# Kernel optimization log

Measured on AMD Instinct MI355X. Metric: run time of the kernel, lower is better.

The kernel has to match this reference:

```python
import jax, jax.numpy as jnp
import numpy as np

NEG_INF = -1e30


def setup_inputs() -> dict:
    B, N, D = 512, 256, 256
    key = jax.random.key(0)
    ks = jax.random.split(key, 10)
    s = 1.0 / np.sqrt(D)
    return {
        "enc": jax.random.normal(ks[0], (B, N, D), dtype=jnp.float32),
        "init_token": jax.random.normal(ks[1], (D,), dtype=jnp.float32),
        "w_ih": jax.random.uniform(ks[2], (3 * D, D), minval=-s, maxval=s, dtype=jnp.float32),
        "w_hh": jax.random.uniform(ks[3], (3 * D, D), minval=-s, maxval=s, dtype=jnp.float32),
        "b_ih": jax.random.uniform(ks[4], (3 * D,), minval=-s, maxval=s, dtype=jnp.float32),
        "b_hh": jax.random.uniform(ks[5], (3 * D,), minval=-s, maxval=s, dtype=jnp.float32),
        "wq": jax.random.uniform(ks[6], (D, D), minval=-s, maxval=s, dtype=jnp.float32),
        "bq": jax.random.uniform(ks[7], (D,), minval=-s, maxval=s, dtype=jnp.float32),
        "wk": jax.random.uniform(ks[8], (D, D), minval=-s, maxval=s, dtype=jnp.float32),
        "bk": jax.random.uniform(ks[9], (D,), minval=-s, maxval=s, dtype=jnp.float32),
    }


def gru_cell(x, h, w_ih, w_hh, b_ih, b_hh):
    # torch.nn.GRUCell math; gates packed as [reset, update, new]
    gi = x @ w_ih.T + b_ih          # [B, 3D]
    gh = h @ w_hh.T + b_hh          # [B, 3D]
    D = h.shape[-1]
    i_r, i_z, i_n = gi[:, :D], gi[:, D:2 * D], gi[:, 2 * D:]
    h_r, h_z, h_n = gh[:, :D], gh[:, D:2 * D], gh[:, 2 * D:]
    r = jax.nn.sigmoid(i_r + h_r)
    z = jax.nn.sigmoid(i_z + h_z)
    n = jnp.tanh(i_n + r * h_n)
    return (1.0 - z) * n + z * h


def pointer_decode(enc, init_token, w_ih, w_hh, b_ih, b_hh, wq, bq, wk, bk):
    # Greedy decode (deterministic analogue of decode_type='greedy').
    B, N, D = enc.shape
    scale = 1.0 / np.sqrt(D)
    keys = enc @ wk.T + bk                         # [B, N, D]
    rows = jnp.arange(B)

    def step(carry, _):
        state, prev_embed, mask = carry
        state = gru_cell(prev_embed, state, w_ih, w_hh, b_ih, b_hh)   # [B, D]
        query = state @ wq.T + bq                                     # [B, D]
        logits = jnp.einsum('bd,bnd->bn', query, keys) * scale        # [B, N]
        logits = jnp.where(mask, logits, NEG_INF)
        logp = jax.nn.log_softmax(logits, axis=-1)                    # [B, N]
        probs = jnp.exp(logp)
        entropy = -jnp.sum(probs * jnp.where(mask, logp, 0.0), axis=-1)  # [B]
        idx = jnp.argmax(probs, axis=-1)                              # [B]
        step_logp = logp[rows, idx]                                   # [B]
        prev_embed = enc[rows, idx]                                   # [B, D]
        mask = mask.at[rows, idx].set(False)
        return (state, prev_embed, mask), (idx, step_logp, entropy)

    carry0 = (enc.mean(axis=1),
              jnp.broadcast_to(init_token, (B, D)),
              jnp.ones((B, N), dtype=bool))
    _, (tours, logps, ents) = jax.lax.scan(step, carry0, None, length=N)
    return tours.T, logps.T, ents.T  # each [B, N]


def reference(enc, init_token, w_ih, w_hh, b_ih, b_hh, wq, bq, wk, bk):
    return pointer_decode(enc, init_token, w_ih, w_hh, b_ih, b_hh, wq, bq, wk, bk)
```

## Files before the change

kernel.cpp:

```cpp
#include <hip/hip_runtime.h>

#define B_ 512
#define N_ 256
#define D_ 256
#define NEGINF (-1e30)

typedef float v4f __attribute__((ext_vector_type(4)));

__global__ void transpose_k(const float* __restrict__ in, float* __restrict__ out,
                            int R, int C) {
  __shared__ float tile[32][33];
  int rb = blockIdx.y * 32, cb = blockIdx.x * 32;
  int tx = threadIdx.x, ty = threadIdx.y;
  for (int i = ty; i < 32; i += 8) {
    int r = rb + i, c = cb + tx;
    if (r < R && c < C) tile[i][tx] = in[r * C + c];
  }
  __syncthreads();
  for (int i = ty; i < 32; i += 8) {
    int c = cb + i, r = rb + tx;
    if (r < R && c < C) out[c * R + r] = tile[tx][i];
  }
}

__global__ __launch_bounds__(256) void packW_k(const float* __restrict__ in,
                                               float* __restrict__ out) {
  int idx = blockIdx.x * 256 + threadIdx.x;
  int j = idx >> 6, c4 = idx & 63;
  int g = j >> 8, o = j & 255;
  int w16 = o >> 4, k = c4 & 15, l = 4 * (o & 15) + (c4 >> 4);
  ((v4f*)out)[((w16 * 16 + k) * 3 + g) * 64 + l] = ((const v4f*)in)[idx];
}

__global__ __launch_bounds__(256) void wqk_k(const float* __restrict__ wk,
                                             const float* __restrict__ wq,
                                             const float* __restrict__ bq,
                                             double* __restrict__ WqkP,
                                             double* __restrict__ bqk) {
  int c = blockIdx.x, e = threadIdx.x;
  double acc = 0.0;
  for (int dd = 0; dd < 256; ++dd)
    acc += (double)wk[dd * 256 + c] * (double)wq[dd * 256 + e];
  int w16 = c >> 4, k2 = (e >> 1) & 31, l = 4 * (c & 15) + (e >> 6), comp = e & 1;
  WqkP[(size_t)(((w16 * 32) + k2) * 64 + l) * 2 + comp] = acc;
  if (e == 0) {
    double s = 0.0;
    for (int dd = 0; dd < 256; ++dd) s += (double)wk[dd * 256 + c] * (double)bq[dd];
    bqk[c] = s;
  }
}

__global__ __launch_bounds__(256) void encp_k(const float* __restrict__ enc,
                                              float* __restrict__ encP) {
  int b = blockIdx.y;
  int idx = blockIdx.x * 256 + threadIdx.x;
  int l = idx & 63, rest = idx >> 6;
  int k = rest & 15, w16 = rest >> 4;
  int n = w16 * 16 + (l >> 2), c4 = (l & 3) * 16 + k;
  ((v4f*)encP)[(size_t)b * 16384 + idx] =
      *(const v4f*)(enc + (size_t)b * 65536 + n * 256 + c4 * 4);
}

__global__ __launch_bounds__(768) void gi_k(const float* __restrict__ enc,
                                            const float* __restrict__ wihT,
                                            const float* __restrict__ b_ih,
                                            double* __restrict__ Gi) {
  int b = blockIdx.x, j = threadIdx.x;
  __shared__ float encS[32][256];
  const float* encB = enc + (size_t)b * 65536;
  double bias = (double)b_ih[j];
  for (int n0 = 0; n0 < 256; n0 += 32) {
    __syncthreads();
    for (int i = j; i < 2048; i += 768)
      ((float4*)encS)[i] = ((const float4*)(encB + n0 * 256))[i];
    __syncthreads();
    double acc[32];
#pragma unroll
    for (int jj = 0; jj < 32; ++jj) acc[jj] = bias;
    for (int c0 = 0; c0 < 256; c0 += 4) {
      double w0 = (double)wihT[(c0 + 0) * 768 + j];
      double w1 = (double)wihT[(c0 + 1) * 768 + j];
      double w2 = (double)wihT[(c0 + 2) * 768 + j];
      double w3 = (double)wihT[(c0 + 3) * 768 + j];
#pragma unroll
      for (int jj = 0; jj < 32; ++jj) {
        const float4 e = *(const float4*)&encS[jj][c0];
        acc[jj] += w0 * (double)e.x + w1 * (double)e.y + w2 * (double)e.z + w3 * (double)e.w;
      }
    }
#pragma unroll
    for (int jj = 0; jj < 32; ++jj)
      Gi[((size_t)b * 256 + n0 + jj) * 768 + j] = acc[jj];
  }
}

template <bool USE_GI>
__global__ __launch_bounds__(1024, 4) void decode_k(
    const float* __restrict__ enc, const float* __restrict__ init_token,
    const float* __restrict__ b_ih, const float* __restrict__ b_hh,
    const float* __restrict__ wihP, const float* __restrict__ whhP,
    const double* __restrict__ WqkP, const double* __restrict__ bqk,
    const float* __restrict__ encP, const double* __restrict__ Gi,
    float* __restrict__ out) {
  const int tid = threadIdx.x;
  const int WV = tid >> 6;
  const int LN = tid & 63;
  const int O = WV * 16 + (LN >> 2);
  const int S = LN & 3;
  const int ROW = S >> 1;
  const int b0 = blockIdx.x * 2;

  __shared__ alignas(16) double hS[2][2][D_];
  __shared__ alignas(16) double xS[2][D_];
  __shared__ alignas(16) double giS[2][768];
  __shared__ alignas(16) double qs[2][D_];
  __shared__ double lg[2][N_];
  __shared__ unsigned char maskS[2][N_];
  __shared__ double redA[16][2], redB[16][2], redC[16][2];
  __shared__ int redI[16][2];

  const float* encB0 = enc + (size_t)b0 * 65536;
  const float* encB1 = encB0 + 65536;
  const v4f* eP0 = (const v4f*)encP + (size_t)b0 * 16384;
  const v4f* eP1 = eP0 + 16384;
  const v4f* wh4 = (const v4f*)whhP;
  const v4f* wi4 = (const v4f*)wihP;
  const double2* Wp2 = (const double2*)WqkP;

  if (tid < 256) xS[0][tid] = (double)init_token[tid];
  {
    double p0 = 0.0, p1 = 0.0;
    const float* e0 = encB0 + (size_t)(S * 64) * 256 + O;
    const float* e1 = encB1 + (size_t)(S * 64) * 256 + O;
#pragma unroll 4
    for (int n = 0; n < 64; ++n) { p0 += (double)e0[n * 256]; p1 += (double)e1[n * 256]; }
    p0 += __shfl_xor(p0, 1); p0 += __shfl_xor(p0, 2);
    p1 += __shfl_xor(p1, 1); p1 += __shfl_xor(p1, 2);
    if (S == 0) { hS[0][0][O] = p0 * (1.0 / 256.0); hS[0][1][O] = p1 * (1.0 / 256.0); }
  }
  if (tid < 256) { maskS[0][tid] = 1; maskS[1][tid] = 1; }
  __syncthreads();
  if (USE_GI) {
    double a0 = 0, a1 = 0, a2 = 0;
#pragma unroll 2
    for (int k = 0; k < 16; ++k) {
      int wb = ((WV * 16 + k) * 3) * 64 + LN;
      v4f ar = wi4[wb], az = wi4[wb + 64], an = wi4[wb + 128];
      const double* xp = &xS[0][S * 64 + 4 * k];
#pragma unroll
      for (int i = 0; i < 4; ++i) {
        a0 += (double)ar[i] * xp[i];
        a1 += (double)az[i] * xp[i];
        a2 += (double)an[i] * xp[i];
      }
    }
    a0 += __shfl_xor(a0, 1); a0 += __shfl_xor(a0, 2);
    a1 += __shfl_xor(a1, 1); a1 += __shfl_xor(a1, 2);
    a2 += __shfl_xor(a2, 1); a2 += __shfl_xor(a2, 2);
    if (S == 0) {
      double v0 = a0 + (double)b_ih[O];
      double v1 = a1 + (double)b_ih[256 + O];
      double v2 = a2 + (double)b_ih[512 + O];
      giS[0][O] = v0;        giS[1][O] = v0;
      giS[0][256 + O] = v1;  giS[1][256 + O] = v1;
      giS[0][512 + O] = v2;  giS[1][512 + O] = v2;
    }
  } else {
    if (tid < 256) xS[1][tid] = xS[0][tid];
  }
  __syncthreads();

  int cur = 0;
  for (int t = 0; t < N_; ++t) {
    const int nxt = cur ^ 1;
    double ghr0 = 0, ghz0 = 0, ghn0 = 0, ghr1 = 0, ghz1 = 0, ghn1 = 0;
    double air0 = 0, aiz0 = 0, ain0 = 0, air1 = 0, aiz1 = 0, ain1 = 0;
#pragma unroll 2
    for (int k = 0; k < 16; ++k) {
      int wb = ((WV * 16 + k) * 3) * 64 + LN;
      v4f br = wh4[wb], bz = wh4[wb + 64], bn = wh4[wb + 128];
      int c = S * 64 + 4 * k;
      const double* h0 = &hS[cur][0][c];
      const double* h1 = &hS[cur][1][c];
#pragma unroll
      for (int i = 0; i < 4; ++i) {
        double wr = (double)br[i], wz = (double)bz[i], wn = (double)bn[i];
        ghr0 += wr * h0[i]; ghz0 += wz * h0[i]; ghn0 += wn * h0[i];
        ghr1 += wr * h1[i]; ghz1 += wz * h1[i]; ghn1 += wn * h1[i];
      }
      if (!USE_GI) {
        v4f ar = wi4[wb], az = wi4[wb + 64], an = wi4[wb + 128];
        const double* x0 = &xS[0][c];
        const double* x1 = &xS[1][c];
#pragma unroll
        for (int i = 0; i < 4; ++i) {
          double wr = (double)ar[i], wz = (double)az[i], wn = (double)an[i];
          air0 += wr * x0[i]; aiz0 += wz * x0[i]; ain0 += wn * x0[i];
          air1 += wr * x1[i]; aiz1 += wz * x1[i]; ain1 += wn * x1[i];
        }
      }
    }
    ghr0 += __shfl_xor(ghr0, 1); ghr0 += __shfl_xor(ghr0, 2);
    ghz0 += __shfl_xor(ghz0, 1); ghz0 += __shfl_xor(ghz0, 2);
    ghn0 += __shfl_xor(ghn0, 1); ghn0 += __shfl_xor(ghn0, 2);
    ghr1 += __shfl_xor(ghr1, 1); ghr1 += __shfl_xor(ghr1, 2);
    ghz1 += __shfl_xor(ghz1, 1); ghz1 += __shfl_xor(ghz1, 2);
    ghn1 += __shfl_xor(ghn1, 1); ghn1 += __shfl_xor(ghn1, 2);
    if (!USE_GI) {
      air0 += __shfl_xor(air0, 1); air0 += __shfl_xor(air0, 2);
      aiz0 += __shfl_xor(aiz0, 1); aiz0 += __shfl_xor(aiz0, 2);
      ain0 += __shfl_xor(ain0, 1); ain0 += __shfl_xor(ain0, 2);
      air1 += __shfl_xor(air1, 1); air1 += __shfl_xor(air1, 2);
      aiz1 += __shfl_xor(aiz1, 1); aiz1 += __shfl_xor(aiz1, 2);
      ain1 += __shfl_xor(ain1, 1); ain1 += __shfl_xor(ain1, 2);
    }
    {
      double gir, giz, gin;
      if (USE_GI) {
        gir = giS[ROW][O]; giz = giS[ROW][256 + O]; gin = giS[ROW][512 + O];
      } else {
        gir = (ROW ? air1 : air0) + (double)b_ih[O];
        giz = (ROW ? aiz1 : aiz0) + (double)b_ih[256 + O];
        gin = (ROW ? ain1 : ain0) + (double)b_ih[512 + O];
      }
      double hr_ = (ROW ? ghr1 : ghr0) + (double)b_hh[O];
      double hz_ = (ROW ? ghz1 : ghz0) + (double)b_hh[256 + O];
      double hn_ = (ROW ? ghn1 : ghn0) + (double)b_hh[512 + O];
      double rr = 1.0 / (1.0 + exp(-(gir + hr_)));
      double zz = 1.0 / (1.0 + exp(-(giz + hz_)));
      double nn = tanh(gin + rr * hn_);
      double hold = hS[cur][ROW][O];
      double hnew = (1.0 - zz) * nn + zz * hold;
      if ((S & 1) == 0) hS[nxt][ROW][O] = hnew;
    }
    __syncthreads();

    {
      double q0 = 0, q1 = 0;
#pragma unroll 4
      for (int k = 0; k < 32; ++k) {
        double2 wv = Wp2[(WV * 32 + k) * 64 + LN];
        int dd = S * 64 + 2 * k;
        q0 += wv.x * hS[nxt][0][dd] + wv.y * hS[nxt][0][dd + 1];
        q1 += wv.x * hS[nxt][1][dd] + wv.y * hS[nxt][1][dd + 1];
      }
      q0 += __shfl_xor(q0, 1); q0 += __shfl_xor(q0, 2);
      q1 += __shfl_xor(q1, 1); q1 += __shfl_xor(q1, 2);
      if (S == 0) { double bb = bqk[O]; qs[0][O] = q0 + bb; qs[1][O] = q1 + bb; }
    }
    __syncthreads();

    double lgv0, lgv1;
    {
      double p0 = 0, p1 = 0;
#pragma unroll 2
      for (int k = 0; k < 16; ++k) {
        int eb = (WV * 16 + k) * 64 + LN;
        v4f e0 = eP0[eb];
        v4f e1 = eP1[eb];
        int c = S * 64 + 4 * k;
        const double* qa = &qs[0][c];
        const double* qb = &qs[1][c];
#pragma unroll
        for (int i = 0; i < 4; ++i) {
          p0 += (double)e0[i] * qa[i];
          p1 += (double)e1[i] * qb[i];
        }
      }
      p0 += __shfl_xor(p0, 1); p0 += __shfl_xor(p0, 2);
      p1 += __shfl_xor(p1, 1); p1 += __shfl_xor(p1, 2);
      lgv0 = 0.0625 * p0; if (!maskS[0][O]) lgv0 = NEGINF;
      lgv1 = 0.0625 * p1; if (!maskS[1][O]) lgv1 = NEGINF;
      if (S == 0) { lg[0][O] = lgv0; lg[1][O] = lgv1; }
      double v0 = lgv0, v1 = lgv1;
      int i0 = O, i1 = O;
#pragma unroll
      for (int off = 1; off < 64; off <<= 1) {
        double t0 = __shfl_xor(v0, off); int ti0 = __shfl_xor(i0, off);
        if (t0 > v0 || (t0 == v0 && ti0 < i0)) { v0 = t0; i0 = ti0; }
        double t1 = __shfl_xor(v1, off); int ti1 = __shfl_xor(i1, off);
        if (t1 > v1 || (t1 == v1 && ti1 < i1)) { v1 = t1; i1 = ti1; }
      }
      if (LN == 0) { redA[WV][0] = v0; redI[WV][0] = i0; redA[WV][1] = v1; redI[WV][1] = i1; }
    }
    __syncthreads();

    double m0 = -1e300, m1 = -1e300;
    int am0 = 0, am1 = 0;
#pragma unroll 4
    for (int w = 0; w < 16; ++w) {
      double va = redA[w][0]; int ia = redI[w][0];
      if (va > m0 || (va == m0 && ia < am0)) { m0 = va; am0 = ia; }
      double vb = redA[w][1]; int ib = redI[w][1];
      if (vb > m1 || (vb == m1 && ib < am1)) { m1 = vb; am1 = ib; }
    }
    {
      double e0 = (S == 0) ? exp(lgv0 - m0) : 0.0;
      double e1 = (S == 0) ? exp(lgv1 - m1) : 0.0;
      double s20 = e0 * (lgv0 - m0);
      double s21 = e1 * (lgv1 - m1);
#pragma unroll
      for (int off = 1; off < 64; off <<= 1) {
        e0 += __shfl_xor(e0, off);
        e1 += __shfl_xor(e1, off);
        s20 += __shfl_xor(s20, off);
        s21 += __shfl_xor(s21, off);
      }
      if (LN == 0) { redB[WV][0] = e0; redB[WV][1] = e1; redC[WV][0] = s20; redC[WV][1] = s21; }
    }
    if (USE_GI) {
      size_t g0 = ((size_t)b0 * 256 + am0) * 768;
      size_t g1 = ((size_t)(b0 + 1) * 256 + am1) * 768;
      if (tid < 768) giS[0][tid] = Gi[g0 + tid];
      int t2 = tid - 256;
      if (t2 >= 0 && t2 < 768) giS[1][t2] = Gi[g1 + t2];
    } else {
      if (tid < 512) {
        int r = tid >> 8, j = tid & 255;
        int am = r ? am1 : am0;
        int c4 = j >> 2;
        int vidx = ((am >> 4) * 16 + (c4 & 15)) * 64 + (4 * (am & 15) + (c4 >> 4));
        const float* ePr = r ? (const float*)eP1 : (const float*)eP0;
        xS[r][j] = (double)ePr[vidx * 4 + (j & 3)];
      }
    }
    __syncthreads();

    if (tid < 2) {
      int r = tid;
      double m = r ? m1 : m0;
      int am = r ? am1 : am0;
      double S1 = 0, S2 = 0;
#pragma unroll 4
      for (int w = 0; w < 16; ++w) { S1 += redB[w][r]; S2 += redC[w][r]; }
      double lS = log(S1);
      double logZ = m + lS;
      size_t row = (size_t)(b0 + r) * N_;
      out[row + t] = (float)am;
      out[(size_t)B_ * N_ + row + t] = (float)(lg[r][am] - logZ);
      out[2 * (size_t)B_ * N_ + row + t] = (float)(lS - S2 / S1);
      maskS[r][am] = 0;
    }
    __syncthreads();
    cur ^= 1;
  }
}

extern "C" void kernel_launch(void* const* d_in, const int* in_sizes, int n_in,
                              void* d_out, int out_size, void* d_ws, size_t ws_size,
                              hipStream_t stream) {
  const float* enc = (const float*)d_in[0];
  const float* init_token = (const float*)d_in[1];
  const float* w_ih = (const float*)d_in[2];
  const float* w_hh = (const float*)d_in[3];
  const float* b_ih = (const float*)d_in[4];
  const float* b_hh = (const float*)d_in[5];
  const float* wq = (const float*)d_in[6];
  const float* bq = (const float*)d_in[7];
  const float* wk = (const float*)d_in[8];
  const float* bk = (const float*)d_in[9];
  (void)bk;
  float* out = (float*)d_out;
  char* wsb = (char*)d_ws;

  float* wihP = (float*)(wsb + 0);
  float* whhP = (float*)(wsb + 786432);
  double* WqkP = (double*)(wsb + 1572864);
  double* bqk = (double*)(wsb + 2097152);
  float* encP = (float*)(wsb + 2099200);
  float* wihT = (float*)(wsb + 136316928);
  double* Gi = (double*)(wsb + 137103360);
  const bool useGi = ws_size >= 942409728ull;

  hipLaunchKernelGGL(packW_k, dim3(192), dim3(256), 0, stream, w_ih, wihP);
  hipLaunchKernelGGL(packW_k, dim3(192), dim3(256), 0, stream, w_hh, whhP);
  hipLaunchKernelGGL(wqk_k, dim3(256), dim3(256), 0, stream, wk, wq, bq, WqkP, bqk);
  hipLaunchKernelGGL(encp_k, dim3(64, 512), dim3(256), 0, stream, enc, encP);
  if (useGi) {
    hipLaunchKernelGGL(transpose_k, dim3(8, 24), dim3(32, 8), 0, stream, w_ih, wihT, 768, 256);
    hipLaunchKernelGGL(gi_k, dim3(512), dim3(768), 0, stream, enc, wihT, b_ih, Gi);
    hipLaunchKernelGGL(decode_k<true>, dim3(B_ / 2), dim3(1024), 0, stream, enc, init_token,
                       b_ih, b_hh, wihP, whhP, WqkP, bqk, encP, Gi, out);
  } else {
    hipLaunchKernelGGL(decode_k<false>, dim3(B_ / 2), dim3(1024), 0, stream, enc, init_token,
                       b_ih, b_hh, wihP, whhP, WqkP, bqk, encP, Gi, out);
  }
}
```

Before: 17.32 ms.

## Drop precomputed Gi table; compute input gates in-loop with padded LDS

New measurement: 17.23 ms. No clear change (-0.5%).

```diff
diff --git a/kernel.cpp b/kernel.cpp
--- a/kernel.cpp
+++ b/kernel.cpp
@@ -5,22 +5,12 @@
 #define D_ 256
 #define NEGINF (-1e30)
 
+#define PD(c) ((c) + ((c) >> 6))
+
 typedef float v4f __attribute__((ext_vector_type(4)));
 
-__global__ void transpose_k(const float* __restrict__ in, float* __restrict__ out,
-                            int R, int C) {
-  __shared__ float tile[32][33];
-  int rb = blockIdx.y * 32, cb = blockIdx.x * 32;
-  int tx = threadIdx.x, ty = threadIdx.y;
-  for (int i = ty; i < 32; i += 8) {
-    int r = rb + i, c = cb + tx;
-    if (r < R && c < C) tile[i][tx] = in[r * C + c];
-  }
-  __syncthreads();
-  for (int i = ty; i < 32; i += 8) {
-    int c = cb + i, r = rb + tx;
-    if (r < R && c < C) out[c * R + r] = tile[tx][i];
-  }
+__device__ __forceinline__ v4f ntload4(const v4f* p) {
+  return __builtin_nontemporal_load(p);
 }
 
 __global__ __launch_bounds__(256) void packW_k(const float* __restrict__ in,
@@ -61,47 +51,12 @@
       *(const v4f*)(enc + (size_t)b * 65536 + n * 256 + c4 * 4);
 }
 
-__global__ __launch_bounds__(768) void gi_k(const float* __restrict__ enc,
-                                            const float* __restrict__ wihT,
-                                            const float* __restrict__ b_ih,
-                                            double* __restrict__ Gi) {
-  int b = blockIdx.x, j = threadIdx.x;
-  __shared__ float encS[32][256];
-  const float* encB = enc + (size_t)b * 65536;
-  double bias = (double)b_ih[j];
-  for (int n0 = 0; n0 < 256; n0 += 32) {
-    __syncthreads();
-    for (int i = j; i < 2048; i += 768)
-      ((float4*)encS)[i] = ((const float4*)(encB + n0 * 256))[i];
-    __syncthreads();
-    double acc[32];
-#pragma unroll
-    for (int jj = 0; jj < 32; ++jj) acc[jj] = bias;
-    for (int c0 = 0; c0 < 256; c0 += 4) {
-      double w0 = (double)wihT[(c0 + 0) * 768 + j];
-      double w1 = (double)wihT[(c0 + 1) * 768 + j];
-      double w2 = (double)wihT[(c0 + 2) * 768 + j];
-      double w3 = (double)wihT[(c0 + 3) * 768 + j];
-#pragma unroll
-      for (int jj = 0; jj < 32; ++jj) {
-        const float4 e = *(const float4*)&encS[jj][c0];
-        acc[jj] += w0 * (double)e.x + w1 * (double)e.y + w2 * (double)e.z + w3 * (double)e.w;
-      }
-    }
-#pragma unroll
-    for (int jj = 0; jj < 32; ++jj)
-      Gi[((size_t)b * 256 + n0 + jj) * 768 + j] = acc[jj];
-  }
-}
-
-template <bool USE_GI>
 __global__ __launch_bounds__(1024, 4) void decode_k(
     const float* __restrict__ enc, const float* __restrict__ init_token,
     const float* __restrict__ b_ih, const float* __restrict__ b_hh,
     const float* __restrict__ wihP, const float* __restrict__ whhP,
     const double* __restrict__ WqkP, const double* __restrict__ bqk,
-    const float* __restrict__ encP, const double* __restrict__ Gi,
-    float* __restrict__ out) {
+    const float* __restrict__ encP, float* __restrict__ out) {
   const int tid = threadIdx.x;
   const int WV = tid >> 6;
   const int LN = tid & 63;
@@ -110,10 +65,9 @@
   const int ROW = S >> 1;
   const int b0 = blockIdx.x * 2;
 
-  __shared__ alignas(16) double hS[2][2][D_];
-  __shared__ alignas(16) double xS[2][D_];
-  __shared__ alignas(16) double giS[2][768];
-  __shared__ alignas(16) double qs[2][D_];
+  __shared__ alignas(16) double hS[2][2][260];
+  __shared__ alignas(16) double xS[2][260];
+  __shared__ alignas(16) double qs[2][260];
   __shared__ double lg[2][N_];
   __shared__ unsigned char maskS[2][N_];
   __shared__ double redA[16][2], redB[16][2], redC[16][2];
@@ -127,7 +81,13 @@
   const v4f* wi4 = (const v4f*)wihP;
   const double2* Wp2 = (const double2*)WqkP;
 
-  if (tid < 256) xS[0][tid] = (double)init_token[tid];
+  if (tid < 256) {
+    double iv = (double)init_token[tid];
+    xS[0][PD(tid)] = iv;
+    xS[1][PD(tid)] = iv;
+    maskS[0][tid] = 1;
+    maskS[1][tid] = 1;
+  }
   {
     double p0 = 0.0, p1 = 0.0;
     const float* e0 = encB0 + (size_t)(S * 64) * 256 + O;
@@ -136,37 +96,10 @@
     for (int n = 0; n < 64; ++n) { p0 += (double)e0[n * 256]; p1 += (double)e1[n * 256]; }
     p0 += __shfl_xor(p0, 1); p0 += __shfl_xor(p0, 2);
     p1 += __shfl_xor(p1, 1); p1 += __shfl_xor(p1, 2);
-    if (S == 0) { hS[0][0][O] = p0 * (1.0 / 256.0); hS[0][1][O] = p1 * (1.0 / 256.0); }
-  }
-  if (tid < 256) { maskS[0][tid] = 1; maskS[1][tid] = 1; }
-  __syncthreads();
-  if (USE_GI) {
-    double a0 = 0, a1 = 0, a2 = 0;
-#pragma unroll 2
-    for (int k = 0; k < 16; ++k) {
-      int wb = ((WV * 16 + k) * 3) * 64 + LN;
-      v4f ar = wi4[wb], az = wi4[wb + 64], an = wi4[wb + 128];
-      const double* xp = &xS[0][S * 64 + 4 * k];
-#pragma unroll
-      for (int i = 0; i < 4; ++i) {
-        a0 += (double)ar[i] * xp[i];
-        a1 += (double)az[i] * xp[i];
-        a2 += (double)an[i] * xp[i];
-      }
-    }
-    a0 += __shfl_xor(a0, 1); a0 += __shfl_xor(a0, 2);
-    a1 += __shfl_xor(a1, 1); a1 += __shfl_xor(a1, 2);
-    a2 += __shfl_xor(a2, 1); a2 += __shfl_xor(a2, 2);
     if (S == 0) {
-      double v0 = a0 + (double)b_ih[O];
-      double v1 = a1 + (double)b_ih[256 + O];
-      double v2 = a2 + (double)b_ih[512 + O];
-      giS[0][O] = v0;        giS[1][O] = v0;
-      giS[0][256 + O] = v1;  giS[1][256 + O] = v1;
-      giS[0][512 + O] = v2;  giS[1][512 + O] = v2;
-    }
-  } else {
-    if (tid < 256) xS[1][tid] = xS[0][tid];
+      hS[0][0][PD(O)] = p0 * (1.0 / 256.0);
+      hS[0][1][PD(O)] = p1 * (1.0 / 256.0);
+    }
   }
   __syncthreads();
 
@@ -175,29 +108,24 @@
     const int nxt = cur ^ 1;
     double ghr0 = 0, ghz0 = 0, ghn0 = 0, ghr1 = 0, ghz1 = 0, ghn1 = 0;
     double air0 = 0, aiz0 = 0, ain0 = 0, air1 = 0, aiz1 = 0, ain1 = 0;
-#pragma unroll 2
+#pragma unroll 4
     for (int k = 0; k < 16; ++k) {
       int wb = ((WV * 16 + k) * 3) * 64 + LN;
       v4f br = wh4[wb], bz = wh4[wb + 64], bn = wh4[wb + 128];
+      v4f ar = wi4[wb], az = wi4[wb + 64], an = wi4[wb + 128];
       int c = S * 64 + 4 * k;
-      const double* h0 = &hS[cur][0][c];
-      const double* h1 = &hS[cur][1][c];
+      const double* h0 = &hS[cur][0][c + S];
+      const double* h1 = &hS[cur][1][c + S];
+      const double* x0 = &xS[0][c + S];
+      const double* x1 = &xS[1][c + S];
 #pragma unroll
       for (int i = 0; i < 4; ++i) {
         double wr = (double)br[i], wz = (double)bz[i], wn = (double)bn[i];
         ghr0 += wr * h0[i]; ghz0 += wz * h0[i]; ghn0 += wn * h0[i];
         ghr1 += wr * h1[i]; ghz1 += wz * h1[i]; ghn1 += wn * h1[i];
-      }
-      if (!USE_GI) {
-        v4f ar = wi4[wb], az = wi4[wb + 64], an = wi4[wb + 128];
-        const double* x0 = &xS[0][c];
-        const double* x1 = &xS[1][c];
-#pragma unroll
-        for (int i = 0; i < 4; ++i) {
-          double wr = (double)ar[i], wz = (double)az[i], wn = (double)an[i];
-          air0 += wr * x0[i]; aiz0 += wz * x0[i]; ain0 += wn * x0[i];
-          air1 += wr * x1[i]; aiz1 += wz * x1[i]; ain1 += wn * x1[i];
-        }
+        double vr = (double)ar[i], vz = (double)az[i], vn = (double)an[i];
+        air0 += vr * x0[i]; aiz0 += vz * x0[i]; ain0 += vn * x0[i];
+        air1 += vr * x1[i]; aiz1 += vz * x1[i]; ain1 += vn * x1[i];
       }
     }
     ghr0 += __shfl_xor(ghr0, 1); ghr0 += __shfl_xor(ghr0, 2);
@@ -206,32 +134,25 @@
     ghr1 += __shfl_xor(ghr1, 1); ghr1 += __shfl_xor(ghr1, 2);
     ghz1 += __shfl_xor(ghz1, 1); ghz1 += __shfl_xor(ghz1, 2);
     ghn1 += __shfl_xor(ghn1, 1); ghn1 += __shfl_xor(ghn1, 2);
-    if (!USE_GI) {
-      air0 += __shfl_xor(air0, 1); air0 += __shfl_xor(air0, 2);
-      aiz0 += __shfl_xor(aiz0, 1); aiz0 += __shfl_xor(aiz0, 2);
-      ain0 += __shfl_xor(ain0, 1); ain0 += __shfl_xor(ain0, 2);
-      air1 += __shfl_xor(air1, 1); air1 += __shfl_xor(air1, 2);
-      aiz1 += __shfl_xor(aiz1, 1); aiz1 += __shfl_xor(aiz1, 2);
-      ain1 += __shfl_xor(ain1, 1); ain1 += __shfl_xor(ain1, 2);
-    }
-    {
-      double gir, giz, gin;
-      if (USE_GI) {
-        gir = giS[ROW][O]; giz = giS[ROW][256 + O]; gin = giS[ROW][512 + O];
-      } else {
-        gir = (ROW ? air1 : air0) + (double)b_ih[O];
-        giz = (ROW ? aiz1 : aiz0) + (double)b_ih[256 + O];
-        gin = (ROW ? ain1 : ain0) + (double)b_ih[512 + O];
-      }
+    air0 += __shfl_xor(air0, 1); air0 += __shfl_xor(air0, 2);
+    aiz0 += __shfl_xor(aiz0, 1); aiz0 += __shfl_xor(aiz0, 2);
+    ain0 += __shfl_xor(ain0, 1); ain0 += __shfl_xor(ain0, 2);
+    air1 += __shfl_xor(air1, 1); air1 += __shfl_xor(air1, 2);
+    aiz1 += __shfl_xor(aiz1, 1); aiz1 += __shfl_xor(aiz1, 2);
+    ain1 += __shfl_xor(ain1, 1); ain1 += __shfl_xor(ain1, 2);
+    {
+      double gir = (ROW ? air1 : air0) + (double)b_ih[O];
+      double giz = (ROW ? aiz1 : aiz0) + (double)b_ih[256 + O];
+      double gin = (ROW ? ain1 : ain0) + (double)b_ih[512 + O];
       double hr_ = (ROW ? ghr1 : ghr0) + (double)b_hh[O];
       double hz_ = (ROW ? ghz1 : ghz0) + (double)b_hh[256 + O];
       double hn_ = (ROW ? ghn1 : ghn0) + (double)b_hh[512 + O];
       double rr = 1.0 / (1.0 + exp(-(gir + hr_)));
       double zz = 1.0 / (1.0 + exp(-(giz + hz_)));
       double nn = tanh(gin + rr * hn_);
-      double hold = hS[cur][ROW][O];
+      double hold = hS[cur][ROW][PD(O)];
       double hnew = (1.0 - zz) * nn + zz * hold;
-      if ((S & 1) == 0) hS[nxt][ROW][O] = hnew;
+      if ((S & 1) == 0) hS[nxt][ROW][PD(O)] = hnew;
     }
     __syncthreads();
 
@@ -241,12 +162,18 @@
       for (int k = 0; k < 32; ++k) {
         double2 wv = Wp2[(WV * 32 + k) * 64 + LN];
         int dd = S * 64 + 2 * k;
-        q0 += wv.x * hS[nxt][0][dd] + wv.y * hS[nxt][0][dd + 1];
-        q1 += wv.x * hS[nxt][1][dd] + wv.y * hS[nxt][1][dd + 1];
+        const double* h0 = &hS[nxt][0][dd + S];
+        const double* h1 = &hS[nxt][1][dd + S];
+        q0 += wv.x * h0[0] + wv.y * h0[1];
+        q1 += wv.x * h1[0] + wv.y * h1[1];
       }
       q0 += __shfl_xor(q0, 1); q0 += __shfl_xor(q0, 2);
       q1 += __shfl_xor(q1, 1); q1 += __shfl_xor(q1, 2);
-      if (S == 0) { double bb = bqk[O]; qs[0][O] = q0 + bb; qs[1][O] = q1 + bb; }
+      if (S == 0) {
+        double bb = bqk[O];
+        qs[0][PD(O)] = q0 + bb;
+        qs[1][PD(O)] = q1 + bb;
+      }
     }
     __syncthreads();
 
@@ -256,11 +183,11 @@
 #pragma unroll 2
       for (int k = 0; k < 16; ++k) {
         int eb = (WV * 16 + k) * 64 + LN;
-        v4f e0 = eP0[eb];
-        v4f e1 = eP1[eb];
+        v4f e0 = ntload4(eP0 + eb);
+        v4f e1 = ntload4(eP1 + eb);
         int c = S * 64 + 4 * k;
-        const double* qa = &qs[0][c];
-        const double* qb = &qs[1][c];
+        const double* qa = &qs[0][c + S];
+        const double* qb = &qs[1][c + S];
 #pragma unroll
         for (int i = 0; i < 4; ++i) {
           p0 += (double)e0[i] * qa[i];
@@ -308,21 +235,13 @@
       }
       if (LN == 0) { redB[WV][0] = e0; redB[WV][1] = e1; redC[WV][0] = s20; redC[WV][1] = s21; }
     }
-    if (USE_GI) {
-      size_t g0 = ((size_t)b0 * 256 + am0) * 768;
-      size_t g1 = ((size_t)(b0 + 1) * 256 + am1) * 768;
-      if (tid < 768) giS[0][tid] = Gi[g0 + tid];
-      int t2 = tid - 256;
-      if (t2 >= 0 && t2 < 768) giS[1][t2] = Gi[g1 + t2];
-    } else {
-      if (tid < 512) {
-        int r = tid >> 8, j = tid & 255;
-        int am = r ? am1 : am0;
-        int c4 = j >> 2;
-        int vidx = ((am >> 4) * 16 + (c4 & 15)) * 64 + (4 * (am & 15) + (c4 >> 4));
-        const float* ePr = r ? (const float*)eP1 : (const float*)eP0;
-        xS[r][j] = (double)ePr[vidx * 4 + (j & 3)];
-      }
+    if (tid < 512) {
+      int r = tid >> 8, j = tid & 255;
+      int am = r ? am1 : am0;
+      int c4 = j >> 2;
+      int vidx = ((am >> 4) * 16 + (c4 & 15)) * 64 + (4 * (am & 15) + (c4 >> 4));
+      const float* ePr = r ? (const float*)eP1 : (const float*)eP0;
+      xS[r][PD(j)] = (double)__builtin_nontemporal_load(ePr + vidx * 4 + (j & 3));
     }
     __syncthreads();
 
@@ -368,21 +287,11 @@
   double* WqkP = (double*)(wsb + 1572864);
   double* bqk = (double*)(wsb + 2097152);
   float* encP = (float*)(wsb + 2099200);
-  float* wihT = (float*)(wsb + 136316928);
-  double* Gi = (double*)(wsb + 137103360);
-  const bool useGi = ws_size >= 942409728ull;
 
   hipLaunchKernelGGL(packW_k, dim3(192), dim3(256), 0, stream, w_ih, wihP);
   hipLaunchKernelGGL(packW_k, dim3(192), dim3(256), 0, stream, w_hh, whhP);
   hipLaunchKernelGGL(wqk_k, dim3(256), dim3(256), 0, stream, wk, wq, bq, WqkP, bqk);
   hipLaunchKernelGGL(encp_k, dim3(64, 512), dim3(256), 0, stream, enc, encP);
-  if (useGi) {
-    hipLaunchKernelGGL(transpose_k, dim3(8, 24), dim3(32, 8), 0, stream, w_ih, wihT, 768, 256);
-    hipLaunchKernelGGL(gi_k, dim3(512), dim3(768), 0, stream, enc, wihT, b_ih, Gi);
-    hipLaunchKernelGGL(decode_k<true>, dim3(B_ / 2), dim3(1024), 0, stream, enc, init_token,
-                       b_ih, b_hh, wihP, whhP, WqkP, bqk, encP, Gi, out);
-  } else {
-    hipLaunchKernelGGL(decode_k<false>, dim3(B_ / 2), dim3(1024), 0, stream, enc, init_token,
-                       b_ih, b_hh, wihP, whhP, WqkP, bqk, encP, Gi, out);
-  }
-}
+  hipLaunchKernelGGL(decode_k, dim3(B_ / 2), dim3(1024), 0, stream, enc, init_token,
+                     b_ih, b_hh, wihP, whhP, WqkP, bqk, encP, out);
+}
```
